# Performance work log

Measured on AMD Instinct MI355X. Metric: run time of the kernel, lower is better.

The kernel has to match this reference:

```python
import jax, jax.numpy as jnp
import numpy as np

GATE_CAP = 15.0
NH = 8
DH = 128  # head_dim = embedding_dim // num_heads
EPS_BACKEND = 1e-6
EPS_NORM = 1e-6


def soft_cap(z, cap):
    return cap * jnp.tanh(z / cap)


def setup_inputs() -> dict:
    key = jax.random.key(0)
    ks = jax.random.split(key, 9)
    B, S, D = 2, 2048, 1024
    s = lambda n: (1.0 / np.sqrt(n)).astype(np.float32) if isinstance(n, np.ndarray) else np.float32(1.0 / np.sqrt(n))
    return {
        "x": jax.random.normal(ks[0], (B, S, D), jnp.float32),
        "Wq": jax.random.normal(ks[1], (D, D), jnp.float32) * s(D),
        "Wk": jax.random.normal(ks[2], (DH, D), jnp.float32) * s(D),
        "Wv": jax.random.normal(ks[3], (DH, D), jnp.float32) * s(D),
        "Wog": jax.random.normal(ks[4], (D, D), jnp.float32) * s(D),
        "Wi": jax.random.normal(ks[5], (NH, D), jnp.float32) * s(D),
        "bi": jnp.zeros((NH,), jnp.float32),
        "Wf": jax.random.normal(ks[6], (NH, D), jnp.float32) * s(D),
        "bf": jnp.ones((NH,), jnp.float32),
        "ln_w": jnp.ones((D,), jnp.float32),
        "Wout": jax.random.normal(ks[7], (D, D), jnp.float32) * s(D),
    }


def reference(x, Wq, Wk, Wv, Wog, Wi, bi, Wf, bf, ln_w, Wout):
    B, S, D = x.shape
    # projections (single weight mode, use_bias=False except gates)
    q = jnp.einsum("bsd,ed->bse", x, Wq).reshape(B, S, NH, DH).transpose(0, 2, 1, 3)  # [B,NH,S,DH]
    k = jnp.einsum("bsd,ed->bse", x, Wk)[:, None, :, :]  # [B,1,S,DH] (num_key_value_heads=1)
    v = jnp.einsum("bsd,ed->bse", x, Wv)[:, None, :, :]
    k = jnp.broadcast_to(k, (B, NH, S, DH))  # repeat_kv
    v = jnp.broadcast_to(v, (B, NH, S, DH))
    o_preact = jnp.einsum("bsd,ed->bse", x, Wog)  # [B,S,D]
    i_pre = soft_cap(jnp.einsum("bsd,hd->bhs", x, Wi) + bi[None, :, None], GATE_CAP)  # [B,NH,S]
    f_pre = soft_cap(jnp.einsum("bsd,hd->bhs", x, Wf) + bf[None, :, None], GATE_CAP)

    # native parallel mLSTM backend (stabilized), no initial state
    log_f = jax.nn.log_sigmoid(f_pre)               # [B,NH,S]
    csum = jnp.cumsum(log_f, axis=-1)
    mat_log_f = csum[:, :, :, None] - csum[:, :, None, :]  # [B,NH,S,S]
    ltr = jnp.tril(jnp.ones((S, S), dtype=bool))
    mat_log_f = jnp.where(ltr, mat_log_f, -jnp.inf)
    mat_log_d = mat_log_f + i_pre[:, :, None, :]
    vec_m = jnp.max(mat_log_d, axis=-1, keepdims=True)      # [B,NH,S,1]
    mat_d = jnp.exp(mat_log_d - vec_m)
    mat_s = jnp.einsum("bhsd,bhtd->bhst", q, k) * (DH ** -0.5)
    mat_c = mat_s * mat_d
    vec_n = jnp.maximum(jnp.abs(jnp.sum(mat_c, axis=-1, keepdims=True)), jnp.exp(-vec_m))
    C = mat_c / (vec_n + EPS_BACKEND)
    h = jnp.einsum("bhst,bhtd->bhsd", C, v)  # [B,NH,S,DH]

    # multihead layernorm (per-head, fp32 reductions, weight only)
    h = h.transpose(0, 2, 1, 3)  # [B,S,NH,DH]
    h32 = h.astype(jnp.float32)
    mu = jnp.mean(h32, axis=-1, keepdims=True)
    var = jnp.mean(jnp.square(h32 - mu), axis=-1, keepdims=True)
    h_norm = ((h32 - mu) * jax.lax.rsqrt(var + EPS_NORM)).astype(h.dtype)
    h_norm = h_norm * ln_w.reshape(NH, DH)[None, None, :, :]
    h_norm = h_norm.reshape(B, S, D)

    h_out = jax.nn.sigmoid(o_preact) * h_norm
    y = jnp.einsum("bsd,ed->bse", h_out, Wout)
    return y
```

## Files before the change

kernel.cpp:

```cpp
#include <hip/hip_runtime.h>


typedef __bf16 bf16x8 __attribute__((ext_vector_type(8)));
typedef float f32x4 __attribute__((ext_vector_type(4)));
typedef unsigned short us8 __attribute__((ext_vector_type(8)));
typedef unsigned short us4 __attribute__((ext_vector_type(4)));

__device__ __forceinline__ unsigned short f2bf(float f) {
    unsigned int u = __builtin_bit_cast(unsigned int, f);
    unsigned int r = u + 0x7fffu + ((u >> 16) & 1u);
    return (unsigned short)(r >> 16);
}
__device__ __forceinline__ float bf2f(unsigned short h) {
    unsigned int u = ((unsigned int)h) << 16;
    return __builtin_bit_cast(float, u);
}
__device__ __forceinline__ f32x4 mfma16(bf16x8 a, bf16x8 b, f32x4 c) {
    return __builtin_amdgcn_mfma_f32_16x16x32_bf16(a, b, c, 0, 0, 0);
}

__global__ __launch_bounds__(256) void k_split_bf16(const float* __restrict__ in,
                                                    unsigned short* __restrict__ hi,
                                                    unsigned short* __restrict__ lo, int n) {
    int i = blockIdx.x * 256 + threadIdx.x;
    if (i < n) {
        float f = in[i];
        unsigned short h = f2bf(f);
        hi[i] = h;
        lo[i] = f2bf(f - bf2f(h));
    }
}

__global__ __launch_bounds__(256) void build_wcat(const float* __restrict__ Wq,
                                                  const float* __restrict__ Wk,
                                                  const float* __restrict__ Wv,
                                                  const float* __restrict__ Wog,
                                                  unsigned short* __restrict__ wh,
                                                  unsigned short* __restrict__ wl) {
    int idx = blockIdx.x * 256 + threadIdx.x;
    if (idx >= 2304 * 1024) return;
    int row = idx >> 10, col = idx & 1023;
    float v;
    if (row < 1024)      v = Wq[(size_t)row * 1024 + col] * 0.08838834764831845f;
    else if (row < 1152) v = Wk[(size_t)(row - 1024) * 1024 + col];
    else if (row < 1280) v = Wv[(size_t)(row - 1152) * 1024 + col];
    else                 v = Wog[(size_t)(row - 1280) * 1024 + col];
    unsigned short h = f2bf(v);
    wh[idx] = h;
    wl[idx] = f2bf(v - bf2f(h));
}

__global__ __launch_bounds__(256) void gates_kernel(const float* __restrict__ x,
                                                    const float* __restrict__ Wi,
                                                    const float* __restrict__ bi,
                                                    const float* __restrict__ Wf,
                                                    const float* __restrict__ bfb,
                                                    float* __restrict__ ipre,
                                                    float* __restrict__ lgf) {
    int bs = blockIdx.x;
    int b = bs >> 11, s = bs & 2047;
    const float* xr = x + (size_t)bs * 1024;
    int lane = threadIdx.x & 63, w = threadIdx.x >> 6;
    const float* W = (w < 2) ? Wi : Wf;
    int h0 = (w & 1) * 4;
    float dot0 = 0.f, dot1 = 0.f, dot2 = 0.f, dot3 = 0.f;
    for (int i = lane; i < 1024; i += 64) {
        float xv = xr[i];
        dot0 += xv * W[(size_t)(h0 + 0) * 1024 + i];
        dot1 += xv * W[(size_t)(h0 + 1) * 1024 + i];
        dot2 += xv * W[(size_t)(h0 + 2) * 1024 + i];
        dot3 += xv * W[(size_t)(h0 + 3) * 1024 + i];
    }
#pragma unroll
    for (int o = 32; o; o >>= 1) {
        dot0 += __shfl_xor(dot0, o);
        dot1 += __shfl_xor(dot1, o);
        dot2 += __shfl_xor(dot2, o);
        dot3 += __shfl_xor(dot3, o);
    }
    if (lane == 0) {
        float d[4] = {dot0, dot1, dot2, dot3};
#pragma unroll
        for (int j = 0; j < 4; j++) {
            int hh = h0 + j;
            if (w < 2) {
                float z = d[j] + bi[hh];
                z = 15.f * tanhf(z * (1.f / 15.f));
                ipre[((size_t)b * 8 + hh) * 2048 + s] = z;
            } else {
                float z = d[j] + bfb[hh];
                z = 15.f * tanhf(z * (1.f / 15.f));
                lgf[((size_t)b * 8 + hh) * 2048 + s] = fminf(z, 0.f) - log1pf(expf(-fabsf(z)));
            }
        }
    }
}

__global__ void scan_kernel(const float* __restrict__ ipre, const float* __restrict__ lgf,
                            float* __restrict__ csum, float* __restrict__ aarr,
                            float* __restrict__ marr) {
    int bh = blockIdx.x;
    int lane = threadIdx.x;
    const float* lf = lgf + (size_t)bh * 2048;
    const float* ip = ipre + (size_t)bh * 2048;
    float* cs = csum + (size_t)bh * 2048;
    float* aa = aarr + (size_t)bh * 2048;
    float* mm = marr + (size_t)bh * 2048;
    float carry = 0.f;
    float carrym = -1e30f;
    for (int c = 0; c < 32; c++) {
        float v = lf[c * 64 + lane];
#pragma unroll
        for (int o = 1; o < 64; o <<= 1) {
            float t = __shfl_up(v, o);
            if (lane >= o) v += t;
        }
        float cval = carry + v;
        cs[c * 64 + lane] = cval;
        float a = ip[c * 64 + lane] - cval;
        aa[c * 64 + lane] = a;
        float mv = a;
#pragma unroll
        for (int o = 1; o < 64; o <<= 1) {
            float t = __shfl_up(mv, o);
            if (lane >= o) mv = fmaxf(mv, t);
        }
        float mval = fmaxf(carrym, mv);
        mm[c * 64 + lane] = mval;
        carry = __shfl(cval, 63);
        carrym = __shfl(mval, 63);
    }
}

__global__ __launch_bounds__(256) void gemm_bt3(const unsigned short* __restrict__ Ah,
                                                const unsigned short* __restrict__ Al,
                                                const unsigned short* __restrict__ Bh,
                                                const unsigned short* __restrict__ Bl,
                                                void* __restrict__ Cp,
                                                unsigned short* __restrict__ Clo,
                                                int K, int ldc, int c_bf16, int og_y0) {
    __shared__ __attribute__((aligned(16))) unsigned short Ash[128 * 40];
    __shared__ __attribute__((aligned(16))) unsigned short Asl[128 * 40];
    __shared__ __attribute__((aligned(16))) unsigned short Bsh[128 * 40];
    __shared__ __attribute__((aligned(16))) unsigned short Bsl[128 * 40];
    const int tid = threadIdx.x;
    const int lane = tid & 63, wv = tid >> 6;
    const int wr = wv >> 1, wc = wv & 1;
    const int fr = lane & 15, fg = lane >> 4;
    const int srow = tid >> 1, scol = (tid & 1) * 16;
    const bool full3 = (blockIdx.y < (unsigned)og_y0);
    const size_t aoff = (size_t)(blockIdx.x * 128 + srow) * K + scol;
    const size_t boff = (size_t)(blockIdx.y * 128 + srow) * K + scol;
    f32x4 acc[4][4] = {};
    us8 avh0, avh1, avl0, avl1, bvh0, bvh1, bvl0, bvl1;
#define GLOAD(KT)                                                              \
    {                                                                          \
        avh0 = *(const us8*)(Ah + aoff + (KT));                                \
        avh1 = *(const us8*)(Ah + aoff + (KT) + 8);                            \
        avl0 = *(const us8*)(Al + aoff + (KT));                                \
        avl1 = *(const us8*)(Al + aoff + (KT) + 8);                            \
        bvh0 = *(const us8*)(Bh + boff + (KT));                                \
        bvh1 = *(const us8*)(Bh + boff + (KT) + 8);                            \
        bvl0 = *(const us8*)(Bl + boff + (KT));                                \
        bvl1 = *(const us8*)(Bl + boff + (KT) + 8);                            \
    }
    GLOAD(0);
    for (int kt = 0; kt < K; kt += 32) {
        __syncthreads();
        *(us8*)&Ash[srow * 40 + scol] = avh0;
        *(us8*)&Ash[srow * 40 + scol + 8] = avh1;
        *(us8*)&Asl[srow * 40 + scol] = avl0;
        *(us8*)&Asl[srow * 40 + scol + 8] = avl1;
        *(us8*)&Bsh[srow * 40 + scol] = bvh0;
        *(us8*)&Bsh[srow * 40 + scol + 8] = bvh1;
        *(us8*)&Bsl[srow * 40 + scol] = bvl0;
        *(us8*)&Bsl[srow * 40 + scol + 8] = bvl1;
        __syncthreads();
        if (kt + 32 < K) GLOAD(kt + 32);
        bf16x8 bfh[4], bfl[4];
#pragma unroll
        for (int j = 0; j < 4; j++) {
            bfh[j] = __builtin_bit_cast(bf16x8, *(const us8*)&Bsh[(64 * wc + 16 * j + fr) * 40 + fg * 8]);
            bfl[j] = __builtin_bit_cast(bf16x8, *(const us8*)&Bsl[(64 * wc + 16 * j + fr) * 40 + fg * 8]);
        }
        __builtin_amdgcn_s_setprio(1);
        if (full3) {
#pragma unroll
            for (int i = 0; i < 4; i++) {
                bf16x8 afh = __builtin_bit_cast(bf16x8, *(const us8*)&Ash[(64 * wr + 16 * i + fr) * 40 + fg * 8]);
                bf16x8 afl = __builtin_bit_cast(bf16x8, *(const us8*)&Asl[(64 * wr + 16 * i + fr) * 40 + fg * 8]);
#pragma unroll
                for (int j = 0; j < 4; j++) {
                    acc[i][j] = mfma16(afh, bfh[j], acc[i][j]);
                    acc[i][j] = mfma16(afh, bfl[j], acc[i][j]);
                    acc[i][j] = mfma16(afl, bfh[j], acc[i][j]);
                }
            }
        } else {
#pragma unroll
            for (int i = 0; i < 4; i++) {
                bf16x8 afh = __builtin_bit_cast(bf16x8, *(const us8*)&Ash[(64 * wr + 16 * i + fr) * 40 + fg * 8]);
#pragma unroll
                for (int j = 0; j < 4; j++)
                    acc[i][j] = mfma16(afh, bfh[j], acc[i][j]);
            }
        }
        __builtin_amdgcn_s_setprio(0);
    }
#undef GLOAD
#pragma unroll
    for (int i = 0; i < 4; i++)
#pragma unroll
        for (int j = 0; j < 4; j++)
#pragma unroll
            for (int e = 0; e < 4; e++) {
                int r = blockIdx.x * 128 + 64 * wr + 16 * i + fg * 4 + e;
                int c = blockIdx.y * 128 + 64 * wc + 16 * j + fr;
                float v = acc[i][j][e];
                if (c_bf16) {
                    unsigned short h = f2bf(v);
                    ((unsigned short*)Cp)[(size_t)r * ldc + c] = h;
                    Clo[(size_t)r * ldc + c] = f2bf(v - bf2f(h));
                } else {
                    ((float*)Cp)[(size_t)r * ldc + c] = v;
                }
            }
}

__global__ __launch_bounds__(256) void make_vt(const unsigned short* __restrict__ ph,
                                               const unsigned short* __restrict__ pl,
                                               unsigned short* __restrict__ vTh,
                                               unsigned short* __restrict__ vTl) {
    __shared__ __attribute__((aligned(16))) unsigned short th[64 * 68];
    __shared__ __attribute__((aligned(16))) unsigned short tl[64 * 68];
    const int bid = blockIdx.x;
    const int st = bid & 31, ct = (bid >> 5) & 1, b = bid >> 6;
    const int tid = threadIdx.x;
    {
        const int sr = tid >> 2, cc = (tid & 3) * 16;
        const size_t rbase = (size_t)(b * 2048 + st * 64 + sr) * 2304 + 1152 + ct * 64 + cc;
        us8 a0 = *(const us8*)(ph + rbase);
        us8 a1 = *(const us8*)(ph + rbase + 8);
        us8 c0 = *(const us8*)(pl + rbase);
        us8 c1 = *(const us8*)(pl + rbase + 8);
        *(us8*)&th[sr * 68 + cc] = a0;
        *(us8*)&th[sr * 68 + cc + 8] = a1;
        *(us8*)&tl[sr * 68 + cc] = c0;
        *(us8*)&tl[sr * 68 + cc + 8] = c1;
    }
    __syncthreads();
    {
        const int cr = tid >> 2, ss = (tid & 3) * 16;
        us8 oh0, oh1, ol0, ol1;
#pragma unroll
        for (int e = 0; e < 8; e++) {
            oh0[e] = th[(ss + e) * 68 + cr];
            oh1[e] = th[(ss + 8 + e) * 68 + cr];
            ol0[e] = tl[(ss + e) * 68 + cr];
            ol1[e] = tl[(ss + 8 + e) * 68 + cr];
        }
        const size_t wbase = (size_t)b * 128 * 2048 + (size_t)(ct * 64 + cr) * 2048 + st * 64 + ss;
        *(us8*)&vTh[wbase] = oh0;
        *(us8*)&vTh[wbase + 8] = oh1;
        *(us8*)&vTl[wbase] = ol0;
        *(us8*)&vTl[wbase + 8] = ol1;
    }
}

__global__ __launch_bounds__(256, 2) void attn_fused(const unsigned short* __restrict__ projh,
                                                     const unsigned short* __restrict__ projl,
                                                     const unsigned short* __restrict__ vTh,
                                                     const unsigned short* __restrict__ vTl,
                                                     const float* __restrict__ aarr,
                                                     const float* __restrict__ marr,
                                                     const float* __restrict__ csum,
                                                     const float* __restrict__ lnw,
                                                     unsigned short* __restrict__ ho_hi,
                                                     unsigned short* __restrict__ ho_lo) {
    __shared__ __attribute__((aligned(16))) unsigned short Klh[2][32 * 148];
    __shared__ __attribute__((aligned(16))) unsigned short Kll[2][32 * 148];
    __shared__ __attribute__((aligned(16))) unsigned short Vlh[2][128 * 40];
    __shared__ __attribute__((aligned(16))) unsigned short Vll[2][128 * 40];
    __shared__ float al[2][32];

    const int idx = blockIdx.x;
    const int half = idx >> 8;
    const int pid = idx & 255;
    const int bh = pid & 15;
    const int qt0 = pid >> 4;
    const int qt = half ? (31 - qt0) : qt0;
    const int b = bh >> 3, h = bh & 7;
    const int tid = threadIdx.x, lane = tid & 63, w = tid >> 6;
    const int fr = lane & 15, fg = lane >> 4;
    const int q0 = qt * 64;
    const int qg = q0 + 16 * w + fr;

    bf16x8 qfh[4], qfl[4];
    {
        const size_t qoff = (size_t)(b * 2048 + qg) * 2304 + h * 128;
#pragma unroll
        for (int ks = 0; ks < 4; ks++) {
            qfh[ks] = __builtin_bit_cast(bf16x8, *(const us8*)(projh + qoff + ks * 32 + fg * 8));
            qfl[ks] = __builtin_bit_cast(bf16x8, *(const us8*)(projl + qoff + ks * 32 + fg * 8));
        }
    }
    const float ma_q = marr[(size_t)bh * 2048 + qg];

    f32x4 acc[8] = {};
    float b_run = 0.f;

    const int kr = tid >> 3, kc = (tid & 7) * 16;
    const int vr = tid >> 1, vc = (tid & 1) * 16;
    const size_t kbase = (size_t)(b * 2048) * 2304 + 1024;
    const size_t vtbase = (size_t)b * 128 * 2048;

    const int nt = 2 * qt + 2;
    us8 kh0, kh1, kl0, kl1, vh0, vh1, vl0, vl1;
    float a_st;
#define LOADT(T0)                                                              \
    {                                                                          \
        const size_t ko = kbase + (size_t)((T0) + kr) * 2304 + kc;             \
        const size_t vo = vtbase + (size_t)vr * 2048 + (T0) + vc;              \
        kh0 = *(const us8*)(projh + ko);                                       \
        kh1 = *(const us8*)(projh + ko + 8);                                   \
        kl0 = *(const us8*)(projl + ko);                                       \
        kl1 = *(const us8*)(projl + ko + 8);                                   \
        vh0 = *(const us8*)(vTh + vo);                                         \
        vh1 = *(const us8*)(vTh + vo + 8);                                     \
        vl0 = *(const us8*)(vTl + vo);                                         \
        vl1 = *(const us8*)(vTl + vo + 8);                                     \
        a_st = (tid < 32) ? aarr[(size_t)bh * 2048 + (T0) + tid] : 0.f;        \
    }
#define STORET(BUF)                                                            \
    {                                                                          \
        *(us8*)&Klh[BUF][kr * 148 + kc] = kh0;                                 \
        *(us8*)&Klh[BUF][kr * 148 + kc + 8] = kh1;                             \
        *(us8*)&Kll[BUF][kr * 148 + kc] = kl0;                                 \
        *(us8*)&Kll[BUF][kr * 148 + kc + 8] = kl1;                             \
        *(us8*)&Vlh[BUF][vr * 40 + vc] = vh0;                                  \
        *(us8*)&Vlh[BUF][vr * 40 + vc + 8] = vh1;                              \
        *(us8*)&Vll[BUF][vr * 40 + vc] = vl0;                                  \
        *(us8*)&Vll[BUF][vr * 40 + vc + 8] = vl1;                              \
        if (tid < 32) al[BUF][tid] = a_st;                                     \
    }

    LOADT(0);
    STORET(0);
    if (nt > 1) LOADT(32);
    __syncthreads();

    for (int kt = 0; kt < nt; kt++) {
        const int cur = kt & 1;
        const int t0 = kt * 32;
        if (kt + 1 < nt) {
            STORET(cur ^ 1);
            if (kt + 2 < nt) LOADT((kt + 2) * 32);
        }

        float dj[2][4];
#pragma unroll
        for (int j = 0; j < 2; j++) {
            f32x4 sfa = {}, sfb = {}, sfc = {};
            __builtin_amdgcn_s_setprio(1);
#pragma unroll
            for (int ks = 0; ks < 4; ks++) {
                bf16x8 kfh = __builtin_bit_cast(bf16x8, *(const us8*)&Klh[cur][(j * 16 + fr) * 148 + ks * 32 + fg * 8]);
                bf16x8 kfl = __builtin_bit_cast(bf16x8, *(const us8*)&Kll[cur][(j * 16 + fr) * 148 + ks * 32 + fg * 8]);
                sfa = mfma16(kfh, qfh[ks], sfa);
                sfb = mfma16(kfh, qfl[ks], sfb);
                sfc = mfma16(kfl, qfh[ks], sfc);
            }
            __builtin_amdgcn_s_setprio(0);
            f32x4 sf = (sfa + sfb) + sfc;
#pragma unroll
            for (int r = 0; r < 4; r++) {
                const int kloc = j * 16 + fg * 4 + r;
                const int key = t0 + kloc;
                const float atv = al[cur][kloc];
                dj[j][r] = (key <= qg) ? sf[r] * __expf(atv - ma_q) : 0.f;
            }
        }

        {
            float ts = dj[0][0] + dj[0][1] + dj[0][2] + dj[0][3]
                     + dj[1][0] + dj[1][1] + dj[1][2] + dj[1][3];
            ts += __shfl_xor(ts, 16);
            ts += __shfl_xor(ts, 32);
            b_run += ts;
        }

        float p8[8];
        const int srlo = 32 * ((lane >> 4) & 1) + fr;
#pragma unroll
        for (int e = 0; e < 8; e++) {
            const int sl = srlo + ((e >= 4) ? 16 : 0);
            const float v0 = __shfl(dj[0][e & 3], sl);
            const float v1 = __shfl(dj[1][e & 3], sl);
            p8[e] = (lane & 32) ? v1 : v0;
        }
        us8 phu, plu;
#pragma unroll
        for (int e = 0; e < 8; e++) {
            unsigned short hh = f2bf(p8[e]);
            phu[e] = hh;
            plu[e] = f2bf(p8[e] - bf2f(hh));
        }
        const bf16x8 pfh = __builtin_bit_cast(bf16x8, phu);
        const bf16x8 pfl = __builtin_bit_cast(bf16x8, plu);

        __builtin_amdgcn_s_setprio(1);
#pragma unroll
        for (int jb = 0; jb < 8; jb++) {
            bf16x8 vfh = __builtin_bit_cast(bf16x8, *(const us8*)&Vlh[cur][(jb * 16 + fr) * 40 + fg * 8]);
            bf16x8 vfl = __builtin_bit_cast(bf16x8, *(const us8*)&Vll[cur][(jb * 16 + fr) * 40 + fg * 8]);
            acc[jb] = mfma16(vfh, pfh, acc[jb]);
            acc[jb] = mfma16(vfh, pfl, acc[jb]);
            acc[jb] = mfma16(vfl, pfh, acc[jb]);
        }
        __builtin_amdgcn_s_setprio(0);
        __syncthreads();
    }
#undef LOADT
#undef STORET

    const float cs_q = csum[(size_t)bh * 2048 + qg];
    const float nf = __expf(-(cs_q + ma_q));
    const float n = fmaxf(fabsf(b_run), nf);
    const float inv = 1.f / (n + 1e-6f);
#pragma unroll
    for (int jb = 0; jb < 8; jb++) acc[jb] *= inv;

    float s1 = 0.f;
#pragma unroll
    for (int jb = 0; jb < 8; jb++) s1 += acc[jb][0] + acc[jb][1] + acc[jb][2] + acc[jb][3];
    s1 += __shfl_xor(s1, 16);
    s1 += __shfl_xor(s1, 32);
    const float mu = s1 * (1.f / 128.f);
    float vv = 0.f;
#pragma unroll
    for (int jb = 0; jb < 8; jb++)
#pragma unroll
        for (int e = 0; e < 4; e++) {
            float d = acc[jb][e] - mu;
            vv += d * d;
        }
    vv += __shfl_xor(vv, 16);
    vv += __shfl_xor(vv, 32);
    const float rstd = rsqrtf(vv * (1.f / 128.f) + 1e-6f);

    const size_t obase = (size_t)(b * 2048 + qg) * 2304 + 1280 + h * 128 + fg * 4;
    const size_t hbase = (size_t)(b * 2048 + qg) * 1024 + h * 128 + fg * 4;
#pragma unroll
    for (int jb = 0; jb < 8; jb++) {
        us4 ogh = *(const us4*)(projh + obase + jb * 16);
        us4 ogl = *(const us4*)(projl + obase + jb * 16);
        f32x4 lw = *(const f32x4*)&lnw[h * 128 + jb * 16 + fg * 4];
        us4 hi4, lo4;
#pragma unroll
        for (int e = 0; e < 4; e++) {
            const float og = bf2f(ogh[e]) + bf2f(ogl[e]);
            const float sig = 1.f / (1.f + __expf(-og));
            const float ho = (acc[jb][e] - mu) * rstd * lw[e] * sig;
            unsigned short h1 = f2bf(ho);
            hi4[e] = h1;
            lo4[e] = f2bf(ho - bf2f(h1));
        }
        *(us4*)&ho_hi[hbase + jb * 16] = hi4;
        *(us4*)&ho_lo[hbase + jb * 16] = lo4;
    }
}

extern "C" void kernel_launch(void* const* d_in, const int* in_sizes, int n_in,
                              void* d_out, int out_size, void* d_ws, size_t ws_size,
                              hipStream_t stream) {
    (void)in_sizes; (void)n_in; (void)out_size; (void)ws_size;
    const float* x    = (const float*)d_in[0];
    const float* Wq   = (const float*)d_in[1];
    const float* Wk   = (const float*)d_in[2];
    const float* Wv   = (const float*)d_in[3];
    const float* Wog  = (const float*)d_in[4];
    const float* Wi   = (const float*)d_in[5];
    const float* bi   = (const float*)d_in[6];
    const float* Wf   = (const float*)d_in[7];
    const float* bfb  = (const float*)d_in[8];
    const float* lnw  = (const float*)d_in[9];
    const float* Wout = (const float*)d_in[10];

    char* p = (char*)d_ws;
    auto carve = [&](size_t bytes) -> char* {
        char* r = p;
        p += (bytes + 255) & ~(size_t)255;
        return r;
    };
    unsigned short* x_hi   = (unsigned short*)carve(4194304ull * 2);
    unsigned short* x_lo   = (unsigned short*)carve(4194304ull * 2);
    unsigned short* wc_hi  = (unsigned short*)carve(2359296ull * 2);
    unsigned short* wc_lo  = (unsigned short*)carve(2359296ull * 2);
    unsigned short* wo_hi  = (unsigned short*)carve(1048576ull * 2);
    unsigned short* wo_lo  = (unsigned short*)carve(1048576ull * 2);
    unsigned short* pr_hi  = (unsigned short*)carve(4096ull * 2304 * 2);
    unsigned short* pr_lo  = (unsigned short*)carve(4096ull * 2304 * 2);
    unsigned short* vT_hi  = (unsigned short*)carve(524288ull * 2);
    unsigned short* vT_lo  = (unsigned short*)carve(524288ull * 2);
    float* ipre    = (float*)carve(32768ull * 4);
    float* lgf_buf = (float*)carve(32768ull * 4);
    float* csum    = (float*)carve(32768ull * 4);
    float* aarr    = (float*)carve(32768ull * 4);
    float* marr    = (float*)carve(32768ull * 4);
    unsigned short* ho_hi = x_hi;
    unsigned short* ho_lo = x_lo;

    k_split_bf16<<<16384, 256, 0, stream>>>(x, x_hi, x_lo, 4194304);
    build_wcat<<<(2359296 + 255) / 256, 256, 0, stream>>>(Wq, Wk, Wv, Wog, wc_hi, wc_lo);
    k_split_bf16<<<4096, 256, 0, stream>>>(Wout, wo_hi, wo_lo, 1048576);
    gates_kernel<<<4096, 256, 0, stream>>>(x, Wi, bi, Wf, bfb, ipre, lgf_buf);
    scan_kernel<<<16, 64, 0, stream>>>(ipre, lgf_buf, csum, aarr, marr);
    gemm_bt3<<<dim3(32, 18), 256, 0, stream>>>(x_hi, x_lo, wc_hi, wc_lo, pr_hi, pr_lo, 1024, 2304, 1, 10);
    make_vt<<<128, 256, 0, stream>>>(pr_hi, pr_lo, vT_hi, vT_lo);
    attn_fused<<<512, 256, 0, stream>>>(pr_hi, pr_lo, vT_hi, vT_lo, aarr, marr, csum, lnw, ho_hi, ho_lo);
    gemm_bt3<<<dim3(32, 8), 256, 0, stream>>>(ho_hi, ho_lo, wo_hi, wo_lo, d_out, nullptr, 1024, 1024, 0, 1000);
}
```

Baseline: 328.8 us.

## Split attention work into 32-query tiles with head-dim split across warps

The attention kernel now processes 32-query tiles instead of 64. Pairs of warps share a query block and each warp accumulates half of the 128-wide output dimension. This doubles the grid to 1024 blocks and halves the accumulator registers so up to four blocks fit per CU. The LDS double buffering is replaced by a single buffer with register prefetch. The layernorm now uses a one-pass sum and sum-of-squares combined across warps through shared memory. The trade-off is that the QK score MFMAs are duplicated across the warp pairs, and each 32-key tile is now loaded for twice as many query tiles.

```diff
diff --git a/kernel.cpp b/kernel.cpp
--- a/kernel.cpp
+++ b/kernel.cpp
@@ -267,7 +267,7 @@
     }
 }
 
-__global__ __launch_bounds__(256, 2) void attn_fused(const unsigned short* __restrict__ projh,
+__global__ __launch_bounds__(256, 4) void attn_fused(const unsigned short* __restrict__ projh,
                                                      const unsigned short* __restrict__ projl,
                                                      const unsigned short* __restrict__ vTh,
                                                      const unsigned short* __restrict__ vTl,
@@ -277,23 +277,24 @@
                                                      const float* __restrict__ lnw,
                                                      unsigned short* __restrict__ ho_hi,
                                                      unsigned short* __restrict__ ho_lo) {
-    __shared__ __attribute__((aligned(16))) unsigned short Klh[2][32 * 148];
-    __shared__ __attribute__((aligned(16))) unsigned short Kll[2][32 * 148];
-    __shared__ __attribute__((aligned(16))) unsigned short Vlh[2][128 * 40];
-    __shared__ __attribute__((aligned(16))) unsigned short Vll[2][128 * 40];
-    __shared__ float al[2][32];
+    __shared__ __attribute__((aligned(16))) unsigned short Klh[32 * 148];
+    __shared__ __attribute__((aligned(16))) unsigned short Kll[32 * 148];
+    __shared__ __attribute__((aligned(16))) unsigned short Vlh[128 * 40];
+    __shared__ __attribute__((aligned(16))) unsigned short Vll[128 * 40];
+    __shared__ float al[32];
+    __shared__ float lnc[2][16][2][2];
 
     const int idx = blockIdx.x;
-    const int half = idx >> 8;
-    const int pid = idx & 255;
-    const int bh = pid & 15;
-    const int qt0 = pid >> 4;
-    const int qt = half ? (31 - qt0) : qt0;
+    const int bh = idx & 15;
+    const int slot = (idx >> 4) & 63;
+    const int qt32 = (slot < 32) ? slot : (95 - slot);
     const int b = bh >> 3, h = bh & 7;
     const int tid = threadIdx.x, lane = tid & 63, w = tid >> 6;
     const int fr = lane & 15, fg = lane >> 4;
-    const int q0 = qt * 64;
-    const int qg = q0 + 16 * w + fr;
+    const int qh = w & 1;
+    const int jbh = w >> 1;
+    const int q0 = qt32 * 32;
+    const int qg = q0 + 16 * qh + fr;
 
     bf16x8 qfh[4], qfl[4];
     {
@@ -306,7 +307,7 @@
     }
     const float ma_q = marr[(size_t)bh * 2048 + qg];
 
-    f32x4 acc[8] = {};
+    f32x4 acc[4] = {};
     float b_run = 0.f;
 
     const int kr = tid >> 3, kc = (tid & 7) * 16;
@@ -314,7 +315,7 @@
     const size_t kbase = (size_t)(b * 2048) * 2304 + 1024;
     const size_t vtbase = (size_t)b * 128 * 2048;
 
-    const int nt = 2 * qt + 2;
+    const int nt = qt32 + 1;
     us8 kh0, kh1, kl0, kl1, vh0, vh1, vl0, vl1;
     float a_st;
 #define LOADT(T0)                                                              \
@@ -331,31 +332,21 @@
         vl1 = *(const us8*)(vTl + vo + 8);                                     \
         a_st = (tid < 32) ? aarr[(size_t)bh * 2048 + (T0) + tid] : 0.f;        \
     }
-#define STORET(BUF)                                                            \
-    {                                                                          \
-        *(us8*)&Klh[BUF][kr * 148 + kc] = kh0;                                 \
-        *(us8*)&Klh[BUF][kr * 148 + kc + 8] = kh1;                             \
-        *(us8*)&Kll[BUF][kr * 148 + kc] = kl0;                                 \
-        *(us8*)&Kll[BUF][kr * 148 + kc + 8] = kl1;                             \
-        *(us8*)&Vlh[BUF][vr * 40 + vc] = vh0;                                  \
-        *(us8*)&Vlh[BUF][vr * 40 + vc + 8] = vh1;                              \
-        *(us8*)&Vll[BUF][vr * 40 + vc] = vl0;                                  \
-        *(us8*)&Vll[BUF][vr * 40 + vc + 8] = vl1;                              \
-        if (tid < 32) al[BUF][tid] = a_st;                                     \
-    }
 
     LOADT(0);
-    STORET(0);
-    if (nt > 1) LOADT(32);
-    __syncthreads();
-
     for (int kt = 0; kt < nt; kt++) {
-        const int cur = kt & 1;
         const int t0 = kt * 32;
-        if (kt + 1 < nt) {
-            STORET(cur ^ 1);
-            if (kt + 2 < nt) LOADT((kt + 2) * 32);
-        }
+        *(us8*)&Klh[kr * 148 + kc] = kh0;
+        *(us8*)&Klh[kr * 148 + kc + 8] = kh1;
+        *(us8*)&Kll[kr * 148 + kc] = kl0;
+        *(us8*)&Kll[kr * 148 + kc + 8] = kl1;
+        *(us8*)&Vlh[vr * 40 + vc] = vh0;
+        *(us8*)&Vlh[vr * 40 + vc + 8] = vh1;
+        *(us8*)&Vll[vr * 40 + vc] = vl0;
+        *(us8*)&Vll[vr * 40 + vc + 8] = vl1;
+        if (tid < 32) al[tid] = a_st;
+        __syncthreads();
+        if (kt + 1 < nt) LOADT(t0 + 32);
 
         float dj[2][4];
 #pragma unroll
@@ -364,8 +355,8 @@
             __builtin_amdgcn_s_setprio(1);
 #pragma unroll
             for (int ks = 0; ks < 4; ks++) {
-                bf16x8 kfh = __builtin_bit_cast(bf16x8, *(const us8*)&Klh[cur][(j * 16 + fr) * 148 + ks * 32 + fg * 8]);
-                bf16x8 kfl = __builtin_bit_cast(bf16x8, *(const us8*)&Kll[cur][(j * 16 + fr) * 148 + ks * 32 + fg * 8]);
+                bf16x8 kfh = __builtin_bit_cast(bf16x8, *(const us8*)&Klh[(j * 16 + fr) * 148 + ks * 32 + fg * 8]);
+                bf16x8 kfl = __builtin_bit_cast(bf16x8, *(const us8*)&Kll[(j * 16 + fr) * 148 + ks * 32 + fg * 8]);
                 sfa = mfma16(kfh, qfh[ks], sfa);
                 sfb = mfma16(kfh, qfl[ks], sfb);
                 sfc = mfma16(kfl, qfh[ks], sfc);
@@ -376,7 +367,7 @@
             for (int r = 0; r < 4; r++) {
                 const int kloc = j * 16 + fg * 4 + r;
                 const int key = t0 + kloc;
-                const float atv = al[cur][kloc];
+                const float atv = al[kloc];
                 dj[j][r] = (key <= qg) ? sf[r] * __expf(atv - ma_q) : 0.f;
             }
         }
@@ -410,48 +401,55 @@
 
         __builtin_amdgcn_s_setprio(1);
 #pragma unroll
-        for (int jb = 0; jb < 8; jb++) {
-            bf16x8 vfh = __builtin_bit_cast(bf16x8, *(const us8*)&Vlh[cur][(jb * 16 + fr) * 40 + fg * 8]);
-            bf16x8 vfl = __builtin_bit_cast(bf16x8, *(const us8*)&Vll[cur][(jb * 16 + fr) * 40 + fg * 8]);
-            acc[jb] = mfma16(vfh, pfh, acc[jb]);
-            acc[jb] = mfma16(vfh, pfl, acc[jb]);
-            acc[jb] = mfma16(vfl, pfh, acc[jb]);
+        for (int jj = 0; jj < 4; jj++) {
+            const int jb = jbh * 4 + jj;
+            bf16x8 vfh = __builtin_bit_cast(bf16x8, *(const us8*)&Vlh[(jb * 16 + fr) * 40 + fg * 8]);
+            bf16x8 vfl = __builtin_bit_cast(bf16x8, *(const us8*)&Vll[(jb * 16 + fr) * 40 + fg * 8]);
+            acc[jj] = mfma16(vfh, pfh, acc[jj]);
+            acc[jj] = mfma16(vfh, pfl, acc[jj]);
+            acc[jj] = mfma16(vfl, pfh, acc[jj]);
         }
         __builtin_amdgcn_s_setprio(0);
         __syncthreads();
     }
 #undef LOADT
-#undef STORET
 
     const float cs_q = csum[(size_t)bh * 2048 + qg];
     const float nf = __expf(-(cs_q + ma_q));
     const float n = fmaxf(fabsf(b_run), nf);
     const float inv = 1.f / (n + 1e-6f);
 #pragma unroll
-    for (int jb = 0; jb < 8; jb++) acc[jb] *= inv;
-
-    float s1 = 0.f;
-#pragma unroll
-    for (int jb = 0; jb < 8; jb++) s1 += acc[jb][0] + acc[jb][1] + acc[jb][2] + acc[jb][3];
+    for (int jj = 0; jj < 4; jj++) acc[jj] *= inv;
+
+    float s1 = 0.f, s2 = 0.f;
+#pragma unroll
+    for (int jj = 0; jj < 4; jj++)
+#pragma unroll
+        for (int e = 0; e < 4; e++) {
+            const float v = acc[jj][e];
+            s1 += v;
+            s2 += v * v;
+        }
     s1 += __shfl_xor(s1, 16);
     s1 += __shfl_xor(s1, 32);
-    const float mu = s1 * (1.f / 128.f);
-    float vv = 0.f;
-#pragma unroll
-    for (int jb = 0; jb < 8; jb++)
-#pragma unroll
-        for (int e = 0; e < 4; e++) {
-            float d = acc[jb][e] - mu;
-            vv += d * d;
-        }
-    vv += __shfl_xor(vv, 16);
-    vv += __shfl_xor(vv, 32);
-    const float rstd = rsqrtf(vv * (1.f / 128.f) + 1e-6f);
+    s2 += __shfl_xor(s2, 16);
+    s2 += __shfl_xor(s2, 32);
+    if (fg == 0) {
+        lnc[qh][fr][jbh][0] = s1;
+        lnc[qh][fr][jbh][1] = s2;
+    }
+    __syncthreads();
+    const float s1t = lnc[qh][fr][0][0] + lnc[qh][fr][1][0];
+    const float s2t = lnc[qh][fr][0][1] + lnc[qh][fr][1][1];
+    const float mu = s1t * (1.f / 128.f);
+    const float var = fmaxf(s2t * (1.f / 128.f) - mu * mu, 0.f);
+    const float rstd = rsqrtf(var + 1e-6f);
 
     const size_t obase = (size_t)(b * 2048 + qg) * 2304 + 1280 + h * 128 + fg * 4;
     const size_t hbase = (size_t)(b * 2048 + qg) * 1024 + h * 128 + fg * 4;
 #pragma unroll
-    for (int jb = 0; jb < 8; jb++) {
+    for (int jj = 0; jj < 4; jj++) {
+        const int jb = jbh * 4 + jj;
         us4 ogh = *(const us4*)(projh + obase + jb * 16);
         us4 ogl = *(const us4*)(projl + obase + jb * 16);
         f32x4 lw = *(const f32x4*)&lnw[h * 128 + jb * 16 + fg * 4];
@@ -460,7 +458,7 @@
         for (int e = 0; e < 4; e++) {
             const float og = bf2f(ogh[e]) + bf2f(ogl[e]);
             const float sig = 1.f / (1.f + __expf(-og));
-            const float ho = (acc[jb][e] - mu) * rstd * lw[e] * sig;
+            const float ho = (acc[jj][e] - mu) * rstd * lw[e] * sig;
             unsigned short h1 = f2bf(ho);
             hi4[e] = h1;
             lo4[e] = f2bf(ho - bf2f(h1));
@@ -517,6 +515,6 @@
     scan_kernel<<<16, 64, 0, stream>>>(ipre, lgf_buf, csum, aarr, marr);
     gemm_bt3<<<dim3(32, 18), 256, 0, stream>>>(x_hi, x_lo, wc_hi, wc_lo, pr_hi, pr_lo, 1024, 2304, 1, 10);
     make_vt<<<128, 256, 0, stream>>>(pr_hi, pr_lo, vT_hi, vT_lo);
-    attn_fused<<<512, 256, 0, stream>>>(pr_hi, pr_lo, vT_hi, vT_lo, aarr, marr, csum, lnw, ho_hi, ho_lo);
+    attn_fused<<<1024, 256, 0, stream>>>(pr_hi, pr_lo, vT_hi, vT_lo, aarr, marr, csum, lnw, ho_hi, ho_lo);
     gemm_bt3<<<dim3(32, 8), 256, 0, stream>>>(ho_hi, ho_lo, wo_hi, wo_lo, d_out, nullptr, 1024, 1024, 0, 1000);
 }
```

New measurement: 426.1 us. +29.6%, slower.

## Split attention PV head dimension across two wave groups with 512-thread blocks

Applied to the files above, without the earlier changes.

Doubles the attn_fused block to 512 threads. Each pair of waves shares the same 16 query rows but owns half of the 128-wide value dimension, which halves per-wave accumulators and tile-load work. The score computation for each query row is now duplicated across both wave halves. The layernorm statistics switch to a single-pass sum and sum-of-squares, combined across the two halves through shared memory behind an extra barrier, which trades some numerical robustness for fewer passes.

```diff
diff --git a/kernel.cpp b/kernel.cpp
--- a/kernel.cpp
+++ b/kernel.cpp
@@ -267,7 +267,7 @@
     }
 }
 
-__global__ __launch_bounds__(256, 2) void attn_fused(const unsigned short* __restrict__ projh,
+__global__ __launch_bounds__(512, 4) void attn_fused(const unsigned short* __restrict__ projh,
                                                      const unsigned short* __restrict__ projl,
                                                      const unsigned short* __restrict__ vTh,
                                                      const unsigned short* __restrict__ vTl,
@@ -292,8 +292,10 @@
     const int b = bh >> 3, h = bh & 7;
     const int tid = threadIdx.x, lane = tid & 63, w = tid >> 6;
     const int fr = lane & 15, fg = lane >> 4;
+    const int qsub = w & 3;
+    const int jbh = w >> 2;
     const int q0 = qt * 64;
-    const int qg = q0 + 16 * w + fr;
+    const int qg = q0 + 16 * qsub + fr;
 
     bf16x8 qfh[4], qfl[4];
     {
@@ -306,41 +308,33 @@
     }
     const float ma_q = marr[(size_t)bh * 2048 + qg];
 
-    f32x4 acc[8] = {};
+    f32x4 acc[4] = {};
     float b_run = 0.f;
 
-    const int kr = tid >> 3, kc = (tid & 7) * 16;
-    const int vr = tid >> 1, vc = (tid & 1) * 16;
+    const int kr = tid >> 4, kc = (tid & 15) * 8;
+    const int vr = tid >> 2, vc = (tid & 3) * 8;
     const size_t kbase = (size_t)(b * 2048) * 2304 + 1024;
     const size_t vtbase = (size_t)b * 128 * 2048;
 
     const int nt = 2 * qt + 2;
-    us8 kh0, kh1, kl0, kl1, vh0, vh1, vl0, vl1;
+    us8 kh0, kl0, vh0, vl0;
     float a_st;
 #define LOADT(T0)                                                              \
     {                                                                          \
         const size_t ko = kbase + (size_t)((T0) + kr) * 2304 + kc;             \
         const size_t vo = vtbase + (size_t)vr * 2048 + (T0) + vc;              \
         kh0 = *(const us8*)(projh + ko);                                       \
-        kh1 = *(const us8*)(projh + ko + 8);                                   \
         kl0 = *(const us8*)(projl + ko);                                       \
-        kl1 = *(const us8*)(projl + ko + 8);                                   \
         vh0 = *(const us8*)(vTh + vo);                                         \
-        vh1 = *(const us8*)(vTh + vo + 8);                                     \
         vl0 = *(const us8*)(vTl + vo);                                         \
-        vl1 = *(const us8*)(vTl + vo + 8);                                     \
         a_st = (tid < 32) ? aarr[(size_t)bh * 2048 + (T0) + tid] : 0.f;        \
     }
 #define STORET(BUF)                                                            \
     {                                                                          \
         *(us8*)&Klh[BUF][kr * 148 + kc] = kh0;                                 \
-        *(us8*)&Klh[BUF][kr * 148 + kc + 8] = kh1;                             \
         *(us8*)&Kll[BUF][kr * 148 + kc] = kl0;                                 \
-        *(us8*)&Kll[BUF][kr * 148 + kc + 8] = kl1;                             \
         *(us8*)&Vlh[BUF][vr * 40 + vc] = vh0;                                  \
-        *(us8*)&Vlh[BUF][vr * 40 + vc + 8] = vh1;                              \
         *(us8*)&Vll[BUF][vr * 40 + vc] = vl0;                                  \
-        *(us8*)&Vll[BUF][vr * 40 + vc + 8] = vl1;                              \
         if (tid < 32) al[BUF][tid] = a_st;                                     \
     }
 
@@ -410,12 +404,13 @@
 
         __builtin_amdgcn_s_setprio(1);
 #pragma unroll
-        for (int jb = 0; jb < 8; jb++) {
+        for (int jj = 0; jj < 4; jj++) {
+            const int jb = jbh * 4 + jj;
             bf16x8 vfh = __builtin_bit_cast(bf16x8, *(const us8*)&Vlh[cur][(jb * 16 + fr) * 40 + fg * 8]);
             bf16x8 vfl = __builtin_bit_cast(bf16x8, *(const us8*)&Vll[cur][(jb * 16 + fr) * 40 + fg * 8]);
-            acc[jb] = mfma16(vfh, pfh, acc[jb]);
-            acc[jb] = mfma16(vfh, pfl, acc[jb]);
-            acc[jb] = mfma16(vfl, pfh, acc[jb]);
+            acc[jj] = mfma16(vfh, pfh, acc[jj]);
+            acc[jj] = mfma16(vfh, pfl, acc[jj]);
+            acc[jj] = mfma16(vfl, pfh, acc[jj]);
         }
         __builtin_amdgcn_s_setprio(0);
         __syncthreads();
@@ -428,30 +423,38 @@
     const float n = fmaxf(fabsf(b_run), nf);
     const float inv = 1.f / (n + 1e-6f);
 #pragma unroll
-    for (int jb = 0; jb < 8; jb++) acc[jb] *= inv;
-
-    float s1 = 0.f;
-#pragma unroll
-    for (int jb = 0; jb < 8; jb++) s1 += acc[jb][0] + acc[jb][1] + acc[jb][2] + acc[jb][3];
+    for (int jj = 0; jj < 4; jj++) acc[jj] *= inv;
+
+    float s1 = 0.f, s2 = 0.f;
+#pragma unroll
+    for (int jj = 0; jj < 4; jj++)
+#pragma unroll
+        for (int e = 0; e < 4; e++) {
+            const float v = acc[jj][e];
+            s1 += v;
+            s2 += v * v;
+        }
     s1 += __shfl_xor(s1, 16);
     s1 += __shfl_xor(s1, 32);
-    const float mu = s1 * (1.f / 128.f);
-    float vv = 0.f;
-#pragma unroll
-    for (int jb = 0; jb < 8; jb++)
-#pragma unroll
-        for (int e = 0; e < 4; e++) {
-            float d = acc[jb][e] - mu;
-            vv += d * d;
-        }
-    vv += __shfl_xor(vv, 16);
-    vv += __shfl_xor(vv, 32);
-    const float rstd = rsqrtf(vv * (1.f / 128.f) + 1e-6f);
+    s2 += __shfl_xor(s2, 16);
+    s2 += __shfl_xor(s2, 32);
+    float* lncp = (float*)&Klh[0][0];
+    if (fg == 0) {
+        lncp[((qsub * 16 + fr) * 2 + jbh) * 2 + 0] = s1;
+        lncp[((qsub * 16 + fr) * 2 + jbh) * 2 + 1] = s2;
+    }
+    __syncthreads();
+    const float s1t = lncp[((qsub * 16 + fr) * 2 + 0) * 2 + 0] + lncp[((qsub * 16 + fr) * 2 + 1) * 2 + 0];
+    const float s2t = lncp[((qsub * 16 + fr) * 2 + 0) * 2 + 1] + lncp[((qsub * 16 + fr) * 2 + 1) * 2 + 1];
+    const float mu = s1t * (1.f / 128.f);
+    const float var = fmaxf(s2t * (1.f / 128.f) - mu * mu, 0.f);
+    const float rstd = rsqrtf(var + 1e-6f);
 
     const size_t obase = (size_t)(b * 2048 + qg) * 2304 + 1280 + h * 128 + fg * 4;
     const size_t hbase = (size_t)(b * 2048 + qg) * 1024 + h * 128 + fg * 4;
 #pragma unroll
-    for (int jb = 0; jb < 8; jb++) {
+    for (int jj = 0; jj < 4; jj++) {
+        const int jb = jbh * 4 + jj;
         us4 ogh = *(const us4*)(projh + obase + jb * 16);
         us4 ogl = *(const us4*)(projl + obase + jb * 16);
         f32x4 lw = *(const f32x4*)&lnw[h * 128 + jb * 16 + fg * 4];
@@ -460,7 +463,7 @@
         for (int e = 0; e < 4; e++) {
             const float og = bf2f(ogh[e]) + bf2f(ogl[e]);
             const float sig = 1.f / (1.f + __expf(-og));
-            const float ho = (acc[jb][e] - mu) * rstd * lw[e] * sig;
+            const float ho = (acc[jj][e] - mu) * rstd * lw[e] * sig;
             unsigned short h1 = f2bf(ho);
             hi4[e] = h1;
             lo4[e] = f2bf(ho - bf2f(h1));
@@ -517,6 +520,6 @@
     scan_kernel<<<16, 64, 0, stream>>>(ipre, lgf_buf, csum, aarr, marr);
     gemm_bt3<<<dim3(32, 18), 256, 0, stream>>>(x_hi, x_lo, wc_hi, wc_lo, pr_hi, pr_lo, 1024, 2304, 1, 10);
     make_vt<<<128, 256, 0, stream>>>(pr_hi, pr_lo, vT_hi, vT_lo);
-    attn_fused<<<512, 256, 0, stream>>>(pr_hi, pr_lo, vT_hi, vT_lo, aarr, marr, csum, lnw, ho_hi, ho_lo);
+    attn_fused<<<512, 512, 0, stream>>>(pr_hi, pr_lo, vT_hi, vT_lo, aarr, marr, csum, lnw, ho_hi, ho_lo);
     gemm_bt3<<<dim3(32, 8), 256, 0, stream>>>(ho_hi, ho_lo, wo_hi, wo_lo, d_out, nullptr, 1024, 1024, 0, 1000);
 }
```

Result: slower. 351.0 us (+6.7%).
